# Kernel tuning notes

Measured on AMD Instinct MI355X. Metric: run time of the kernel, lower is better.

Reference implementation:

```python
import jax, jax.numpy as jnp
import numpy as np

N, E, DIN, D, H = 10000, 160000, 256, 64, 8
HC = D * H  # 512

def _p(key, shape, fan_in):
    return jax.random.normal(key, shape, dtype=jnp.float32) * (1.0 / np.sqrt(fan_in))

def setup_inputs() -> dict:
    key = jax.random.key(0)
    k = iter(jax.random.split(key, 64))
    inp = {}
    inp['x'] = jax.random.normal(next(k), (N, DIN), dtype=jnp.float32)
    inp['edge_index'] = jax.random.randint(next(k), (2, E), 0, N, dtype=jnp.int64)
    inp['Wp'] = _p(next(k), (DIN, D), DIN); inp['bp'] = jnp.zeros((D,), jnp.float32)
    # layer 0: in=D -> H*D
    for nm in ['Wq0', 'Wk0', 'Wv0', 'Ws0']:
        inp[nm] = _p(next(k), (D, HC), D)
    for nm in ['bq0', 'bk0', 'bv0', 'bs0']:
        inp[nm] = jnp.zeros((HC,), jnp.float32)
    # layers 1..4 stacked: in=HC -> HC
    for nm in ['Wq', 'Wk', 'Wv', 'Ws']:
        inp[nm] = _p(next(k), (4, HC, HC), HC)
    for nm in ['bq', 'bk', 'bv', 'bs']:
        inp[nm] = jnp.zeros((4, HC), jnp.float32)
    # final conv: in=HC -> D, heads=1, concat=False
    for nm in ['Wqf', 'Wkf', 'Wvf', 'Wsf']:
        inp[nm] = _p(next(k), (HC, D), HC)
    for nm in ['bqf', 'bkf', 'bvf', 'bsf']:
        inp[nm] = jnp.zeros((D,), jnp.float32)
    inp['Wc1'] = _p(next(k), (D, D // 2), D); inp['bc1'] = jnp.zeros((D // 2,), jnp.float32)
    inp['Wc2'] = _p(next(k), (D // 2, 2), D // 2); inp['bc2'] = jnp.zeros((2,), jnp.float32)
    return inp

def _tconv(x, src, dst, Wq, bq, Wk, bk, Wv, bv, Ws, bs, heads, concat):
    n = x.shape[0]
    c = Wq.shape[1] // heads
    q = (x @ Wq + bq).reshape(n, heads, c)
    kk = (x @ Wk + bk).reshape(n, heads, c)
    v = (x @ Wv + bv).reshape(n, heads, c)
    scale = 1.0 / jnp.sqrt(jnp.asarray(c, x.dtype))
    alpha = jnp.einsum('ehc,ehc->eh', q[dst], kk[src]) * scale  # [E,H]
    amax = jax.ops.segment_max(alpha, dst, num_segments=n)
    ex = jnp.exp(alpha - amax[dst])
    denom = jax.ops.segment_sum(ex, dst, num_segments=n)
    w = ex / denom[dst]  # segment softmax over incoming edges
    agg = jax.ops.segment_sum(w[:, :, None] * v[src], dst, num_segments=n)  # [N,H,C]
    skip = x @ Ws + bs
    if concat:
        return agg.reshape(n, heads * c) + skip
    return agg.mean(axis=1) + skip

def reference(x, edge_index, Wp, bp, Wq0, bq0, Wk0, bk0, Wv0, bv0, Ws0, bs0,
              Wq, bq, Wk, bk, Wv, bv, Ws, bs,
              Wqf, bqf, Wkf, bkf, Wvf, bvf, Wsf, bsf,
              Wc1, bc1, Wc2, bc2):
    src, dst = edge_index[0], edge_index[1]
    h = x @ Wp + bp
    h = jax.nn.relu(_tconv(h, src, dst, Wq0, bq0, Wk0, bk0, Wv0, bv0, Ws0, bs0, H, True))
    for l in range(4):
        h = jax.nn.relu(_tconv(h, src, dst, Wq[l], bq[l], Wk[l], bk[l], Wv[l], bv[l], Ws[l], bs[l], H, True))
    h = _tconv(h, src, dst, Wqf, bqf, Wkf, bkf, Wvf, bvf, Wsf, bsf, 1, False)
    g = h.mean(axis=0, keepdims=True)  # batch=None path: [1,D]
    logits = jax.nn.relu(g @ Wc1 + bc1) @ Wc2 + bc2
    return logits
```

## Files before the change

kernel.cpp:

```cpp
#include <hip/hip_runtime.h>
#include <hip/hip_bf16.h>
#include <cstddef>
#include <cstdint>

static inline int cdiv(int a, int b) { return (a + b - 1) / b; }

typedef short short8v __attribute__((ext_vector_type(8)));
typedef float float4v __attribute__((ext_vector_type(4)));

__device__ inline unsigned short f2b(float f) {
    union { float f; unsigned u; } x; x.f = f;
    unsigned u = x.u;
    return (unsigned short)((u + 0x7fff + ((u >> 16) & 1)) >> 16);
}

__device__ inline float lo2f(unsigned u) { union { unsigned x; float f; } c; c.x = u << 16; return c.f; }
__device__ inline float hi2f(unsigned u) { union { unsigned x; float f; } c; c.x = u & 0xffff0000u; return c.f; }
__device__ inline float b2f(unsigned short b) {
    union { unsigned u; float f; } x; x.u = ((unsigned)b) << 16;
    return x.f;
}

__device__ __forceinline__ void u4tof8(uint4 u, float* f) {
    f[0] = lo2f(u.x); f[1] = hi2f(u.x); f[2] = lo2f(u.y); f[3] = hi2f(u.y);
    f[4] = lo2f(u.z); f[5] = hi2f(u.z); f[6] = lo2f(u.w); f[7] = hi2f(u.w);
}

__device__ __forceinline__ void gload_lds16(const unsigned short* g, unsigned short* lds) {
    __builtin_amdgcn_global_load_lds(
        (const __attribute__((address_space(1))) unsigned int*)g,
        (__attribute__((address_space(3))) unsigned int*)lds, 16, 0, 0);
}


__global__ void count_kernel(const int* __restrict__ ei, int* __restrict__ indeg, int E) {
    int e = blockIdx.x * blockDim.x + threadIdx.x;
    if (e < E) atomicAdd(&indeg[ei[E + e]], 1);
}

__global__ void scan_kernel(const int* __restrict__ indeg, int* __restrict__ offs, int n) {
    __shared__ int tmp[1024];
    __shared__ int carry_s;
    int t = threadIdx.x;
    if (t == 0) { carry_s = 0; offs[0] = 0; }
    __syncthreads();
    for (int base = 0; base < n; base += 1024) {
        int i = base + t;
        int v = (i < n) ? indeg[i] : 0;
        tmp[t] = v;
        __syncthreads();
        for (int d = 1; d < 1024; d <<= 1) {
            int add = (t >= d) ? tmp[t - d] : 0;
            __syncthreads();
            tmp[t] += add;
            __syncthreads();
        }
        if (i < n) offs[i + 1] = carry_s + tmp[t];
        __syncthreads();
        if (t == 0) carry_s += tmp[1023];
        __syncthreads();
    }
}

__global__ void fill_kernel(const int* __restrict__ ei, const int* __restrict__ offs,
                            int* __restrict__ cursor, int* __restrict__ csrc, int E) {
    int e = blockIdx.x * blockDim.x + threadIdx.x;
    if (e < E) {
        int d = ei[E + e];
        int s = ei[e];
        int pos = atomicAdd(&cursor[d], 1);
        csrc[offs[d] + pos] = s;
    }
}


__global__ void f2b_kernel(const float* __restrict__ in, unsigned short* __restrict__ out, int n4) {
    int stride = gridDim.x * blockDim.x;
    for (int i = blockIdx.x * blockDim.x + threadIdx.x; i < n4; i += stride) {
        float4 v = reinterpret_cast<const float4*>(in)[i];
        ushort4 o;
        o.x = f2b(v.x); o.y = f2b(v.y); o.z = f2b(v.z); o.w = f2b(v.w);
        reinterpret_cast<ushort4*>(out)[i] = o;
    }
}

__global__ void transpose_b16_kernel(const float* __restrict__ Wq, const float* __restrict__ Wk,
                                     const float* __restrict__ Wv, const float* __restrict__ Ws,
                                     unsigned short* __restrict__ out) {
    const int K = 512, Nc = 512;
    int z = blockIdx.z;
    int which = z & 3;
    const float* W = (which == 0) ? Wq : (which == 1) ? Wk : (which == 2) ? Wv : Ws;
    W += (size_t)(z >> 2) * K * Nc;
    unsigned short* Wt = out + (size_t)z * K * Nc;
    __shared__ float t[32][33];
    int k0 = blockIdx.x * 32, c0 = blockIdx.y * 32;
    int tx = threadIdx.x, ty = threadIdx.y;
    #pragma unroll
    for (int i = 0; i < 32; i += 8) t[ty + i][tx] = W[(size_t)(k0 + ty + i) * Nc + c0 + tx];
    __syncthreads();
    #pragma unroll
    for (int i = 0; i < 32; i += 8) Wt[(size_t)(c0 + ty + i) * K + k0 + tx] = f2b(t[tx][ty + i]);
}

struct SmallT {
    const float* src[9];
    unsigned short* dst[9];
    int rows[9];
    int cols[9];
};

__global__ void transpose_small_kernel(SmallT p) {
    int mat = blockIdx.y;
    int rows = p.rows[mat], cols = p.cols[mat];
    int tilesC = cols >> 5;
    int tiles = (rows >> 5) * tilesC;
    if ((int)blockIdx.x >= tiles) return;
    int tr = blockIdx.x / tilesC, tc = blockIdx.x % tilesC;
    const float* src = p.src[mat];
    unsigned short* dst = p.dst[mat];
    __shared__ float t[32][33];
    int r0 = tr * 32, c0 = tc * 32;
    int tx = threadIdx.x, ty = threadIdx.y;
    #pragma unroll
    for (int i = 0; i < 32; i += 8) t[ty + i][tx] = src[(size_t)(r0 + ty + i) * cols + c0 + tx];
    __syncthreads();
    #pragma unroll
    for (int i = 0; i < 32; i += 8) dst[(size_t)(c0 + ty + i) * rows + r0 + tx] = f2b(t[tx][ty + i]);
}


struct GemmPtrs {
    const unsigned short* B[4];
    const float* bias[4];
    void* C[4];
    int bf16[4];
};

__global__ __launch_bounds__(256) void mfma_gemm4(const unsigned short* __restrict__ A,
                                                  GemmPtrs p, int M, int nb) {
    __shared__ unsigned short As[128 * 32];
    __shared__ unsigned short Bs[128 * 32];
    int i = blockIdx.x;
    int wk = (nb & 7) ? i : ((i & 7) * (nb >> 3) + (i >> 3));
    int xt = wk >> 4, yt = wk & 15;
    int row0 = xt * 128;
    int wsel = yt >> 2;
    int col0 = (yt & 3) * 128;
    const unsigned short* Bt = p.B[wsel];

    int tid = threadIdx.x;
    int lane = tid & 63;
    int w = tid >> 6;
    int wr = w >> 1, wc = w & 1;
    float4v acc[4][4] = {};

    int c0i = w * 2;
    int srow = c0i * 16 + (lane >> 2);
    int scol = (lane & 3) * 8;

    const unsigned short* Abase = A + (size_t)row0 * 512;
    const unsigned short* Bbase = Bt + (size_t)col0 * 512;

    for (int k0 = 0; k0 < 512; k0 += 32) {
        gload_lds16(Abase + (size_t)srow * 512 + k0 + scol, &As[c0i * 512]);
        gload_lds16(Abase + (size_t)(srow + 16) * 512 + k0 + scol, &As[(c0i + 1) * 512]);
        gload_lds16(Bbase + (size_t)srow * 512 + k0 + scol, &Bs[c0i * 512]);
        gload_lds16(Bbase + (size_t)(srow + 16) * 512 + k0 + scol, &Bs[(c0i + 1) * 512]);
        __syncthreads();
        int r16 = lane & 15;
        int kc = (lane >> 4) * 8;
        short8v af[4], bf[4];
        #pragma unroll
        for (int mi = 0; mi < 4; ++mi)
            af[mi] = *reinterpret_cast<const short8v*>(&As[(wr * 64 + mi * 16 + r16) * 32 + kc]);
        #pragma unroll
        for (int nj = 0; nj < 4; ++nj)
            bf[nj] = *reinterpret_cast<const short8v*>(&Bs[(wc * 64 + nj * 16 + r16) * 32 + kc]);
        #pragma unroll
        for (int mi = 0; mi < 4; ++mi)
            #pragma unroll
            for (int nj = 0; nj < 4; ++nj)
                acc[mi][nj] = __builtin_amdgcn_mfma_f32_16x16x32_bf16(af[mi], bf[nj], acc[mi][nj], 0, 0, 0);
        __syncthreads();
    }

    const float* bias = p.bias[wsel];
    int outbf = p.bf16[wsel];
    float* Cf = (float*)p.C[wsel];
    unsigned short* Cb = (unsigned short*)p.C[wsel];
    int crow_base = row0 + wr * 64 + (lane >> 4) * 4;
    int ccol_base = col0 + wc * 64 + (lane & 15);
    #pragma unroll
    for (int mi = 0; mi < 4; ++mi) {
        #pragma unroll
        for (int r = 0; r < 4; ++r) {
            int grow = crow_base + mi * 16 + r;
            if (grow >= M) continue;
            #pragma unroll
            for (int nj = 0; nj < 4; ++nj) {
                int gcol = ccol_base + nj * 16;
                float val = acc[mi][nj][r] + bias[gcol];
                if (outbf) Cb[(size_t)grow * 512 + gcol] = f2b(val);
                else       Cf[(size_t)grow * 512 + gcol] = val;
            }
        }
    }
}


__global__ __launch_bounds__(256) void mfma_flex(const unsigned short* __restrict__ A,
                                                 GemmPtrs p, int M, int K, int Nc) {
    __shared__ unsigned short As[128][40];
    __shared__ unsigned short Bs[64][40];
    int tid = threadIdx.x;
    int lane = tid & 63;
    int w = tid >> 6;
    int row0 = blockIdx.x * 128;
    int nb = Nc >> 6;
    int wsel = blockIdx.y / nb;
    int col0 = (blockIdx.y % nb) * 64;
    const unsigned short* Bt = p.B[wsel];

    float4v acc[2][4] = {};

    int ra = tid >> 1;
    int ca = (tid & 1) * 16;
    int rb = tid >> 2;
    int cb = (tid & 3) * 8;

    for (int k0 = 0; k0 < K; k0 += 32) {
        {
            int grow = row0 + ra;
            uint4 a0 = make_uint4(0u, 0u, 0u, 0u), a1 = make_uint4(0u, 0u, 0u, 0u);
            if (grow < M) {
                a0 = *reinterpret_cast<const uint4*>(&A[(size_t)grow * K + k0 + ca]);
                a1 = *reinterpret_cast<const uint4*>(&A[(size_t)grow * K + k0 + ca + 8]);
            }
            *reinterpret_cast<uint4*>(&As[ra][ca]) = a0;
            *reinterpret_cast<uint4*>(&As[ra][ca + 8]) = a1;
            uint4 bv = *reinterpret_cast<const uint4*>(&Bt[(size_t)(col0 + rb) * K + k0 + cb]);
            *reinterpret_cast<uint4*>(&Bs[rb][cb]) = bv;
        }
        __syncthreads();
        short8v af[2], bf[4];
        int r16 = lane & 15;
        int kc = (lane >> 4) * 8;
        #pragma unroll
        for (int mi = 0; mi < 2; ++mi)
            af[mi] = *reinterpret_cast<const short8v*>(&As[w * 32 + mi * 16 + r16][kc]);
        #pragma unroll
        for (int nj = 0; nj < 4; ++nj)
            bf[nj] = *reinterpret_cast<const short8v*>(&Bs[nj * 16 + r16][kc]);
        #pragma unroll
        for (int mi = 0; mi < 2; ++mi)
            #pragma unroll
            for (int nj = 0; nj < 4; ++nj)
                acc[mi][nj] = __builtin_amdgcn_mfma_f32_16x16x32_bf16(af[mi], bf[nj], acc[mi][nj], 0, 0, 0);
        __syncthreads();
    }

    const float* bias = p.bias[wsel];
    int outbf = p.bf16[wsel];
    float* Cf = (float*)p.C[wsel];
    unsigned short* Cb = (unsigned short*)p.C[wsel];
    int crow_base = row0 + w * 32 + (lane >> 4) * 4;
    int ccol_base = col0 + (lane & 15);
    #pragma unroll
    for (int mi = 0; mi < 2; ++mi) {
        #pragma unroll
        for (int r = 0; r < 4; ++r) {
            int grow = crow_base + mi * 16 + r;
            if (grow >= M) continue;
            #pragma unroll
            for (int nj = 0; nj < 4; ++nj) {
                int gcol = ccol_base + nj * 16;
                float val = acc[mi][nj][r] + bias[gcol];
                if (outbf) Cb[(size_t)grow * Nc + gcol] = f2b(val);
                else       Cf[(size_t)grow * Nc + gcol] = val;
            }
        }
    }
}


__global__ __launch_bounds__(256) void agg8_kernel(const unsigned short* __restrict__ q,
                                                   const unsigned short* __restrict__ kb,
                                                   const unsigned short* __restrict__ vb,
                                                   const unsigned short* __restrict__ skip,
                                                   const int* __restrict__ offs, const int* __restrict__ csrc,
                                                   unsigned short* __restrict__ outb, int N) {
    int lane = threadIdx.x & 63;
    int node = blockIdx.x * (blockDim.x >> 6) + (threadIdx.x >> 6);
    if (node >= N) return;

    size_t rbase = (size_t)node * 512 + lane * 8;
    float qv[8];
    u4tof8(*reinterpret_cast<const uint4*>(&q[rbase]), qv);

    int e0 = offs[node], e1 = offs[node + 1];
    float m = -3.4e38f, wsum = 0.f;
    float accv[8] = {};

    int s = e0;
    for (; s + 2 <= e1; s += 2) {
        int src0 = csrc[s], src1 = csrc[s + 1];
        size_t b0 = (size_t)src0 * 512 + lane * 8;
        size_t b1 = (size_t)src1 * 512 + lane * 8;
        uint4 k0 = *reinterpret_cast<const uint4*>(&kb[b0]);
        uint4 k1 = *reinterpret_cast<const uint4*>(&kb[b1]);
        uint4 v0 = *reinterpret_cast<const uint4*>(&vb[b0]);
        uint4 v1 = *reinterpret_cast<const uint4*>(&vb[b1]);
        float kk0[8], kk1[8], vv0[8], vv1[8];
        u4tof8(k0, kk0); u4tof8(k1, kk1); u4tof8(v0, vv0); u4tof8(v1, vv1);
        float d0 = 0.f, d1 = 0.f;
        #pragma unroll
        for (int j = 0; j < 8; ++j) { d0 += qv[j] * kk0[j]; d1 += qv[j] * kk1[j]; }
        d0 += __shfl_xor(d0, 1); d1 += __shfl_xor(d1, 1);
        d0 += __shfl_xor(d0, 2); d1 += __shfl_xor(d1, 2);
        d0 += __shfl_xor(d0, 4); d1 += __shfl_xor(d1, 4);
        float a0 = d0 * 0.125f, a1 = d1 * 0.125f;
        float mnew = fmaxf(m, fmaxf(a0, a1));
        float corr = __expf(m - mnew);
        float x0 = __expf(a0 - mnew);
        float x1 = __expf(a1 - mnew);
        wsum = wsum * corr + x0 + x1;
        #pragma unroll
        for (int j = 0; j < 8; ++j) accv[j] = accv[j] * corr + x0 * vv0[j] + x1 * vv1[j];
        m = mnew;
    }
    if (s < e1) {
        int src0 = csrc[s];
        size_t b0 = (size_t)src0 * 512 + lane * 8;
        float kk0[8], vv0[8];
        u4tof8(*reinterpret_cast<const uint4*>(&kb[b0]), kk0);
        u4tof8(*reinterpret_cast<const uint4*>(&vb[b0]), vv0);
        float d0 = 0.f;
        #pragma unroll
        for (int j = 0; j < 8; ++j) d0 += qv[j] * kk0[j];
        d0 += __shfl_xor(d0, 1);
        d0 += __shfl_xor(d0, 2);
        d0 += __shfl_xor(d0, 4);
        float a0 = d0 * 0.125f;
        float mnew = fmaxf(m, a0);
        float corr = __expf(m - mnew);
        float x0 = __expf(a0 - mnew);
        wsum = wsum * corr + x0;
        #pragma unroll
        for (int j = 0; j < 8; ++j) accv[j] = accv[j] * corr + x0 * vv0[j];
        m = mnew;
    }

    float inv = (e1 > e0) ? (1.0f / wsum) : 0.f;
    float sk[8];
    u4tof8(*reinterpret_cast<const uint4*>(&skip[rbase]), sk);
    ushort4 o0, o1;
    o0.x = f2b(fmaxf(sk[0] + accv[0] * inv, 0.f));
    o0.y = f2b(fmaxf(sk[1] + accv[1] * inv, 0.f));
    o0.z = f2b(fmaxf(sk[2] + accv[2] * inv, 0.f));
    o0.w = f2b(fmaxf(sk[3] + accv[3] * inv, 0.f));
    o1.x = f2b(fmaxf(sk[4] + accv[4] * inv, 0.f));
    o1.y = f2b(fmaxf(sk[5] + accv[5] * inv, 0.f));
    o1.z = f2b(fmaxf(sk[6] + accv[6] * inv, 0.f));
    o1.w = f2b(fmaxf(sk[7] + accv[7] * inv, 0.f));
    *reinterpret_cast<ushort4*>(&outb[rbase]) = o0;
    *reinterpret_cast<ushort4*>(&outb[rbase + 4]) = o1;
}


__global__ __launch_bounds__(256) void aggf_kernel(const unsigned short* __restrict__ q,
                                                   const unsigned short* __restrict__ kb,
                                                   const unsigned short* __restrict__ vb,
                                                   const int* __restrict__ offs, const int* __restrict__ csrc,
                                                   float* __restrict__ out, int N) {
    const int HC = 64;
    int lane = threadIdx.x & 63;
    int node = blockIdx.x * (blockDim.x >> 6) + (threadIdx.x >> 6);
    if (node >= N) return;
    int g = lane >> 4;
    int r = lane & 15;

    size_t qbase = (size_t)node * HC + 4 * r;
    ushort4 q4u = *reinterpret_cast<const ushort4*>(&q[qbase]);
    float q4[4] = {b2f(q4u.x), b2f(q4u.y), b2f(q4u.z), b2f(q4u.w)};

    int e0 = offs[node], e1 = offs[node + 1];
    float m = -3.4e38f, wsum = 0.f;
    float accv[4] = {0.f, 0.f, 0.f, 0.f};

    int nIt = (e1 - e0 + 3) >> 2;
    for (int it = 0; it < nIt; ++it) {
        int s = e0 + it * 4 + g;
        bool valid = s < e1;
        int src = csrc[valid ? s : (e1 - 1)];
        size_t base = (size_t)src * HC + 4 * r;
        ushort4 k4 = *reinterpret_cast<const ushort4*>(&kb[base]);
        float d = q4[0] * b2f(k4.x) + q4[1] * b2f(k4.y) + q4[2] * b2f(k4.z) + q4[3] * b2f(k4.w);
        d += __shfl_xor(d, 1);
        d += __shfl_xor(d, 2);
        d += __shfl_xor(d, 4);
        d += __shfl_xor(d, 8);
        float alpha = valid ? d * 0.125f : -3.4e38f;
        float am = fmaxf(alpha, __shfl_xor(alpha, 16));
        am = fmaxf(am, __shfl_xor(am, 32));
        float mnew = fmaxf(m, am);
        float corr = __expf(m - mnew);
        float ex = __expf(alpha - mnew);
        ushort4 v4 = *reinterpret_cast<const ushort4*>(&vb[base]);
        wsum = wsum * corr + ex;
        accv[0] = accv[0] * corr + ex * b2f(v4.x);
        accv[1] = accv[1] * corr + ex * b2f(v4.y);
        accv[2] = accv[2] * corr + ex * b2f(v4.z);
        accv[3] = accv[3] * corr + ex * b2f(v4.w);
        m = mnew;
    }

    #pragma unroll
    for (int off = 16; off <= 32; off <<= 1) {
        wsum += __shfl_xor(wsum, off);
        #pragma unroll
        for (int j = 0; j < 4; ++j) accv[j] += __shfl_xor(accv[j], off);
    }

    if (g == 0) {
        float inv = (e1 > e0) ? (1.0f / wsum) : 0.f;
        float4 o = *reinterpret_cast<const float4*>(&out[qbase]);
        o.x += accv[0] * inv;
        o.y += accv[1] * inv;
        o.z += accv[2] * inv;
        o.w += accv[3] * inv;
        *reinterpret_cast<float4*>(&out[qbase]) = o;
    }
}


__global__ void pool_kernel(const float* __restrict__ hin, float* __restrict__ g, int N) {
    int dim = blockIdx.x;
    float s = 0.f;
    for (int i = threadIdx.x; i < N; i += blockDim.x) s += hin[(size_t)i * 64 + dim];
    __shared__ float red[256];
    red[threadIdx.x] = s;
    __syncthreads();
    for (int d = 128; d >= 1; d >>= 1) {
        if ((int)threadIdx.x < d) red[threadIdx.x] += red[threadIdx.x + d];
        __syncthreads();
    }
    if (threadIdx.x == 0) g[dim] = red[0] / (float)N;
}

__global__ void mlp_kernel(const float* __restrict__ g, const float* __restrict__ Wc1,
                           const float* __restrict__ bc1, const float* __restrict__ Wc2,
                           const float* __restrict__ bc2, float* __restrict__ out) {
    __shared__ float gs[64];
    __shared__ float h1[32];
    int t = threadIdx.x;
    if (t < 64) gs[t] = g[t];
    __syncthreads();
    if (t < 32) {
        float s = bc1[t];
        for (int i = 0; i < 64; ++i) s += gs[i] * Wc1[i * 32 + t];
        h1[t] = fmaxf(s, 0.f);
    }
    __syncthreads();
    if (t < 2) {
        float s = bc2[t];
        for (int i = 0; i < 32; ++i) s += h1[i] * Wc2[i * 2 + t];
        out[t] = s;
    }
}


extern "C" void kernel_launch(void* const* d_in, const int* in_sizes, int n_in,
                              void* d_out, int out_size, void* d_ws, size_t ws_size,
                              hipStream_t stream) {
    const float* x   = (const float*)d_in[0];
    const int*   ei  = (const int*)d_in[1];
    const float* Wp  = (const float*)d_in[2];
    const float* bp  = (const float*)d_in[3];
    const float* Wq0 = (const float*)d_in[4];
    const float* Wk0 = (const float*)d_in[5];
    const float* Wv0 = (const float*)d_in[6];
    const float* Ws0 = (const float*)d_in[7];
    const float* bq0 = (const float*)d_in[8];
    const float* bk0 = (const float*)d_in[9];
    const float* bv0 = (const float*)d_in[10];
    const float* bs0 = (const float*)d_in[11];
    const float* Wq  = (const float*)d_in[12];
    const float* Wk  = (const float*)d_in[13];
    const float* Wv  = (const float*)d_in[14];
    const float* Ws  = (const float*)d_in[15];
    const float* bq  = (const float*)d_in[16];
    const float* bk  = (const float*)d_in[17];
    const float* bv  = (const float*)d_in[18];
    const float* bs  = (const float*)d_in[19];
    const float* Wqf = (const float*)d_in[20];
    const float* Wkf = (const float*)d_in[21];
    const float* Wvf = (const float*)d_in[22];
    const float* Wsf = (const float*)d_in[23];
    const float* bqf = (const float*)d_in[24];
    const float* bkf = (const float*)d_in[25];
    const float* bvf = (const float*)d_in[26];
    const float* bsf = (const float*)d_in[27];
    const float* Wc1 = (const float*)d_in[28];
    const float* bc1 = (const float*)d_in[29];
    const float* Wc2 = (const float*)d_in[30];
    const float* bc2 = (const float*)d_in[31];

    const int N = in_sizes[0] / 256;
    const int E = in_sizes[1] / 2;
    const int HC = 512;

    size_t NB = (size_t)N * HC;
    const size_t WSMALL = 64 * 256 + 8 * 512 * 64;
    size_t need = 6 * NB * sizeof(unsigned short)
                + (size_t)16 * 512 * 512 * sizeof(unsigned short)
                + WSMALL * sizeof(unsigned short)
                + NB * sizeof(float)
                + (size_t)(2 * N + 1 + E) * sizeof(int)
                + 64 * sizeof(float) + 4096;
    if (ws_size < need) return;

    unsigned short* h0    = (unsigned short*)d_ws;
    unsigned short* h1    = h0 + NB;
    unsigned short* qb16  = h1 + NB;
    unsigned short* kb    = qb16 + NB;
    unsigned short* vb    = kb + NB;
    unsigned short* skipb = vb + NB;
    unsigned short* wt16  = skipb + NB;
    unsigned short* wsm   = wt16 + (size_t)16 * 512 * 512;
    uintptr_t pa = (uintptr_t)(wsm + WSMALL);
    pa = (pa + 255) & ~(uintptr_t)255;
    float* hf32 = (float*)pa;
    int* offs   = (int*)(hf32 + NB);
    int* cursor = offs + (N + 1);
    int* csrc   = cursor + N;
    float* gbuf = (float*)(csrc + E);
    unsigned short* xb = qb16;

    hipMemsetAsync(cursor, 0, sizeof(int) * N, stream);
    count_kernel<<<cdiv(E, 256), 256, 0, stream>>>(ei, cursor, E);
    scan_kernel<<<1, 1024, 0, stream>>>(cursor, offs, N);
    hipMemsetAsync(cursor, 0, sizeof(int) * N, stream);
    fill_kernel<<<cdiv(E, 256), 256, 0, stream>>>(ei, offs, cursor, csrc, E);

    transpose_b16_kernel<<<dim3(16, 16, 16), dim3(32, 8), 0, stream>>>(Wq, Wk, Wv, Ws, wt16);
    {
        SmallT st;
        unsigned short* wp_t = wsm;
        unsigned short* w0_t = wsm + 64 * 256;
        unsigned short* wf_t = w0_t + 4 * 512 * 64;
        st.src[0] = Wp;  st.dst[0] = wp_t; st.rows[0] = 256; st.cols[0] = 64;
        const float* w0s[4] = {Wq0, Wk0, Wv0, Ws0};
        const float* wfs[4] = {Wqf, Wkf, Wvf, Wsf};
        for (int i = 0; i < 4; ++i) {
            st.src[1 + i] = w0s[i]; st.dst[1 + i] = w0_t + i * 512 * 64;
            st.rows[1 + i] = 64; st.cols[1 + i] = 512;
            st.src[5 + i] = wfs[i]; st.dst[5 + i] = wf_t + i * 64 * 512;
            st.rows[5 + i] = 512; st.cols[5 + i] = 64;
        }
        transpose_small_kernel<<<dim3(32, 9), dim3(32, 8), 0, stream>>>(st);
    }

    f2b_kernel<<<1280, 256, 0, stream>>>(x, xb, N * 256 / 4);
    {
        GemmPtrs gp;
        gp.B[0] = wsm; gp.bias[0] = bp; gp.C[0] = h0; gp.bf16[0] = 1;
        gp.B[1] = gp.B[2] = gp.B[3] = wsm; gp.bias[1] = gp.bias[2] = gp.bias[3] = bp;
        gp.C[1] = gp.C[2] = gp.C[3] = h0; gp.bf16[1] = gp.bf16[2] = gp.bf16[3] = 1;
        mfma_flex<<<dim3(cdiv(N, 128), 1), 256, 0, stream>>>(xb, gp, N, 256, 64);
    }

    {
        GemmPtrs gp;
        unsigned short* w0_t = wsm + 64 * 256;
        gp.B[0] = w0_t + 0 * 512 * 64; gp.bias[0] = bq0; gp.C[0] = qb16;  gp.bf16[0] = 1;
        gp.B[1] = w0_t + 1 * 512 * 64; gp.bias[1] = bk0; gp.C[1] = kb;    gp.bf16[1] = 1;
        gp.B[2] = w0_t + 2 * 512 * 64; gp.bias[2] = bv0; gp.C[2] = vb;    gp.bf16[2] = 1;
        gp.B[3] = w0_t + 3 * 512 * 64; gp.bias[3] = bs0; gp.C[3] = skipb; gp.bf16[3] = 1;
        mfma_flex<<<dim3(cdiv(N, 128), 4 * 8), 256, 0, stream>>>(h0, gp, N, 64, 512);
    }
    agg8_kernel<<<cdiv(N, 4), 256, 0, stream>>>(qb16, kb, vb, skipb, offs, csrc, h1, N);

    unsigned short* hcur = h1;
    unsigned short* hnext = h0;
    int gx = cdiv(N, 128);
    for (int l = 0; l < 4; ++l) {
        GemmPtrs gp;
        gp.B[0] = wt16 + (size_t)(l * 4 + 0) * 512 * 512;
        gp.B[1] = wt16 + (size_t)(l * 4 + 1) * 512 * 512;
        gp.B[2] = wt16 + (size_t)(l * 4 + 2) * 512 * 512;
        gp.B[3] = wt16 + (size_t)(l * 4 + 3) * 512 * 512;
        gp.bias[0] = bq + l * HC;
        gp.bias[1] = bk + l * HC;
        gp.bias[2] = bv + l * HC;
        gp.bias[3] = bs + l * HC;
        gp.C[0] = qb16; gp.C[1] = kb; gp.C[2] = vb; gp.C[3] = skipb;
        gp.bf16[0] = 1; gp.bf16[1] = 1; gp.bf16[2] = 1; gp.bf16[3] = 1;
        mfma_gemm4<<<gx * 16, 256, 0, stream>>>(hcur, gp, N, gx * 16);
        agg8_kernel<<<cdiv(N, 4), 256, 0, stream>>>(qb16, kb, vb, skipb, offs, csrc, hnext, N);
        { unsigned short* t = hcur; hcur = hnext; hnext = t; }
    }

    {
        GemmPtrs gp;
        unsigned short* wf_t = wsm + 64 * 256 + 4 * 512 * 64;
        gp.B[0] = wf_t + 0 * 64 * 512; gp.bias[0] = bqf; gp.C[0] = qb16; gp.bf16[0] = 1;
        gp.B[1] = wf_t + 1 * 64 * 512; gp.bias[1] = bkf; gp.C[1] = kb;   gp.bf16[1] = 1;
        gp.B[2] = wf_t + 2 * 64 * 512; gp.bias[2] = bvf; gp.C[2] = vb;   gp.bf16[2] = 1;
        gp.B[3] = wf_t + 3 * 64 * 512; gp.bias[3] = bsf; gp.C[3] = hf32; gp.bf16[3] = 0;
        mfma_flex<<<dim3(cdiv(N, 128), 4), 256, 0, stream>>>(hcur, gp, N, 512, 64);
    }
    aggf_kernel<<<cdiv(N, 4), 256, 0, stream>>>(qb16, kb, vb, offs, csrc, hf32, N);

    pool_kernel<<<64, 256, 0, stream>>>(hf32, gbuf, N);
    mlp_kernel<<<1, 64, 0, stream>>>(gbuf, Wc1, bc1, Wc2, bc2, (float*)d_out);
}
```

Before: 595.9 us.

## Load GEMM fragments directly from global into registers with prefetch, drop LDS staging

The mfma_gemm4 kernel no longer stages A/B tiles through LDS with barriers. Each lane now loads its MFMA fragments straight from global memory, double-buffering the next k-slice in registers while the current MFMAs run. This removes the two barriers and the LDS round trip per k-step. In exchange, data shared between waves is loaded redundantly from global/L2, and the loads are strided 16-byte accesses per row, which are less coalesced.

```diff
diff --git a/kernel.cpp b/kernel.cpp
--- a/kernel.cpp
+++ b/kernel.cpp
@@ -24,12 +24,6 @@
 __device__ __forceinline__ void u4tof8(uint4 u, float* f) {
     f[0] = lo2f(u.x); f[1] = hi2f(u.x); f[2] = lo2f(u.y); f[3] = hi2f(u.y);
     f[4] = lo2f(u.z); f[5] = hi2f(u.z); f[6] = lo2f(u.w); f[7] = hi2f(u.w);
-}
-
-__device__ __forceinline__ void gload_lds16(const unsigned short* g, unsigned short* lds) {
-    __builtin_amdgcn_global_load_lds(
-        (const __attribute__((address_space(1))) unsigned int*)g,
-        (__attribute__((address_space(3))) unsigned int*)lds, 16, 0, 0);
 }
 
 
@@ -139,8 +133,6 @@
 
 __global__ __launch_bounds__(256) void mfma_gemm4(const unsigned short* __restrict__ A,
                                                   GemmPtrs p, int M, int nb) {
-    __shared__ unsigned short As[128 * 32];
-    __shared__ unsigned short Bs[128 * 32];
     int i = blockIdx.x;
     int wk = (nb & 7) ? i : ((i & 7) * (nb >> 3) + (i >> 3));
     int xt = wk >> 4, yt = wk & 15;
@@ -153,36 +145,44 @@
     int lane = tid & 63;
     int w = tid >> 6;
     int wr = w >> 1, wc = w & 1;
+    int r16 = lane & 15;
+    int kc = (lane >> 4) * 8;
+
     float4v acc[4][4] = {};
 
-    int c0i = w * 2;
-    int srow = c0i * 16 + (lane >> 2);
-    int scol = (lane & 3) * 8;
-
-    const unsigned short* Abase = A + (size_t)row0 * 512;
-    const unsigned short* Bbase = Bt + (size_t)col0 * 512;
+    const unsigned short* Ap[4];
+    const unsigned short* Bp[4];
+    #pragma unroll
+    for (int t = 0; t < 4; ++t) {
+        int ra = row0 + wr * 64 + t * 16 + r16;
+        if (ra >= M) ra = M - 1;
+        Ap[t] = A + (size_t)ra * 512 + kc;
+        Bp[t] = Bt + (size_t)(col0 + wc * 64 + t * 16 + r16) * 512 + kc;
+    }
+
+    short8v a_[4], b_[4], an[4], bn[4];
+    #pragma unroll
+    for (int t = 0; t < 4; ++t) {
+        a_[t] = *reinterpret_cast<const short8v*>(Ap[t]);
+        b_[t] = *reinterpret_cast<const short8v*>(Bp[t]);
+    }
 
     for (int k0 = 0; k0 < 512; k0 += 32) {
-        gload_lds16(Abase + (size_t)srow * 512 + k0 + scol, &As[c0i * 512]);
-        gload_lds16(Abase + (size_t)(srow + 16) * 512 + k0 + scol, &As[(c0i + 1) * 512]);
-        gload_lds16(Bbase + (size_t)srow * 512 + k0 + scol, &Bs[c0i * 512]);
-        gload_lds16(Bbase + (size_t)(srow + 16) * 512 + k0 + scol, &Bs[(c0i + 1) * 512]);
-        __syncthreads();
-        int r16 = lane & 15;
-        int kc = (lane >> 4) * 8;
-        short8v af[4], bf[4];
-        #pragma unroll
-        for (int mi = 0; mi < 4; ++mi)
-            af[mi] = *reinterpret_cast<const short8v*>(&As[(wr * 64 + mi * 16 + r16) * 32 + kc]);
-        #pragma unroll
-        for (int nj = 0; nj < 4; ++nj)
-            bf[nj] = *reinterpret_cast<const short8v*>(&Bs[(wc * 64 + nj * 16 + r16) * 32 + kc]);
+        int nxt = k0 + 32;
+        if (nxt < 512) {
+            #pragma unroll
+            for (int t = 0; t < 4; ++t) {
+                an[t] = *reinterpret_cast<const short8v*>(Ap[t] + nxt);
+                bn[t] = *reinterpret_cast<const short8v*>(Bp[t] + nxt);
+            }
+        }
         #pragma unroll
         for (int mi = 0; mi < 4; ++mi)
             #pragma unroll
             for (int nj = 0; nj < 4; ++nj)
-                acc[mi][nj] = __builtin_amdgcn_mfma_f32_16x16x32_bf16(af[mi], bf[nj], acc[mi][nj], 0, 0, 0);
-        __syncthreads();
+                acc[mi][nj] = __builtin_amdgcn_mfma_f32_16x16x32_bf16(a_[mi], b_[nj], acc[mi][nj], 0, 0, 0);
+        #pragma unroll
+        for (int t = 0; t < 4; ++t) { a_[t] = an[t]; b_[t] = bn[t]; }
     }
 
     const float* bias = p.bias[wsel];
```

New measurement: 829.1 us. 39.1% more time.

## Store K/V head-major and aggregate per head with four edges per wave

Applied to the files above, without the earlier changes.

The GEMM epilogues now write K and V in head-major layout ([head][node][64]). The attention aggregation is split so each wave handles one (node, head) pair, processing four edges in parallel across 16-lane groups. Per-head K/V tables are smaller, so gathers should get better cache locality per head, and there are eight times as many blocks for parallelism. In exchange, Q and skip reads are repeated per head, the epilogue stores become strided, and extra shuffles are needed to merge the four edge groups.

```diff
diff --git a/kernel.cpp b/kernel.cpp
--- a/kernel.cpp
+++ b/kernel.cpp
@@ -135,10 +135,11 @@
     const float* bias[4];
     void* C[4];
     int bf16[4];
+    int hm[4];
 };
 
 __global__ __launch_bounds__(256) void mfma_gemm4(const unsigned short* __restrict__ A,
-                                                  GemmPtrs p, int M, int nb) {
+                                                  GemmPtrs p, int M, int nb, int kvN) {
     __shared__ unsigned short As[128 * 32];
     __shared__ unsigned short Bs[128 * 32];
     int i = blockIdx.x;
@@ -187,10 +188,12 @@
 
     const float* bias = p.bias[wsel];
     int outbf = p.bf16[wsel];
+    int hm = p.hm[wsel];
     float* Cf = (float*)p.C[wsel];
     unsigned short* Cb = (unsigned short*)p.C[wsel];
     int crow_base = row0 + wr * 64 + (lane >> 4) * 4;
     int ccol_base = col0 + wc * 64 + (lane & 15);
+    int headbase = (col0 + wc * 64) >> 6;
     #pragma unroll
     for (int mi = 0; mi < 4; ++mi) {
         #pragma unroll
@@ -201,8 +204,13 @@
             for (int nj = 0; nj < 4; ++nj) {
                 int gcol = ccol_base + nj * 16;
                 float val = acc[mi][nj][r] + bias[gcol];
-                if (outbf) Cb[(size_t)grow * 512 + gcol] = f2b(val);
-                else       Cf[(size_t)grow * 512 + gcol] = val;
+                if (hm) {
+                    Cb[((size_t)headbase * kvN + grow) * 64 + (gcol & 63)] = f2b(val);
+                } else if (outbf) {
+                    Cb[(size_t)grow * 512 + gcol] = f2b(val);
+                } else {
+                    Cf[(size_t)grow * 512 + gcol] = val;
+                }
             }
         }
     }
@@ -210,7 +218,7 @@
 
 
 __global__ __launch_bounds__(256) void mfma_flex(const unsigned short* __restrict__ A,
-                                                 GemmPtrs p, int M, int K, int Nc) {
+                                                 GemmPtrs p, int M, int K, int Nc, int kvN) {
     __shared__ unsigned short As[128][40];
     __shared__ unsigned short Bs[64][40];
     int tid = threadIdx.x;
@@ -262,10 +270,12 @@
 
     const float* bias = p.bias[wsel];
     int outbf = p.bf16[wsel];
+    int hm = p.hm[wsel];
     float* Cf = (float*)p.C[wsel];
     unsigned short* Cb = (unsigned short*)p.C[wsel];
     int crow_base = row0 + w * 32 + (lane >> 4) * 4;
     int ccol_base = col0 + (lane & 15);
+    int headbase = col0 >> 6;
     #pragma unroll
     for (int mi = 0; mi < 2; ++mi) {
         #pragma unroll
@@ -276,95 +286,87 @@
             for (int nj = 0; nj < 4; ++nj) {
                 int gcol = ccol_base + nj * 16;
                 float val = acc[mi][nj][r] + bias[gcol];
-                if (outbf) Cb[(size_t)grow * Nc + gcol] = f2b(val);
-                else       Cf[(size_t)grow * Nc + gcol] = val;
+                if (hm) {
+                    Cb[((size_t)headbase * kvN + grow) * 64 + (gcol & 63)] = f2b(val);
+                } else if (outbf) {
+                    Cb[(size_t)grow * Nc + gcol] = f2b(val);
+                } else {
+                    Cf[(size_t)grow * Nc + gcol] = val;
+                }
             }
         }
     }
 }
 
 
-__global__ __launch_bounds__(256) void agg8_kernel(const unsigned short* __restrict__ q,
-                                                   const unsigned short* __restrict__ kb,
-                                                   const unsigned short* __restrict__ vb,
-                                                   const unsigned short* __restrict__ skip,
-                                                   const int* __restrict__ offs, const int* __restrict__ csrc,
-                                                   unsigned short* __restrict__ outb, int N) {
+__global__ __launch_bounds__(256) void agg8h_kernel(const unsigned short* __restrict__ q,
+                                                    const unsigned short* __restrict__ kb,
+                                                    const unsigned short* __restrict__ vb,
+                                                    const unsigned short* __restrict__ skip,
+                                                    const int* __restrict__ offs, const int* __restrict__ csrc,
+                                                    unsigned short* __restrict__ outb, int N) {
+    int head = blockIdx.x & 7;
+    int node = (blockIdx.x >> 3) * (blockDim.x >> 6) + (threadIdx.x >> 6);
+    if (node >= N) return;
     int lane = threadIdx.x & 63;
-    int node = blockIdx.x * (blockDim.x >> 6) + (threadIdx.x >> 6);
-    if (node >= N) return;
-
-    size_t rbase = (size_t)node * 512 + lane * 8;
-    float qv[8];
-    u4tof8(*reinterpret_cast<const uint4*>(&q[rbase]), qv);
+    int g = lane >> 4;
+    int r = lane & 15;
+
+    size_t qoff = (size_t)node * 512 + head * 64 + 4 * r;
+    ushort4 q4u = *reinterpret_cast<const ushort4*>(&q[qoff]);
+    float q4[4] = {b2f(q4u.x), b2f(q4u.y), b2f(q4u.z), b2f(q4u.w)};
+
+    const unsigned short* kh = kb + (size_t)head * N * 64;
+    const unsigned short* vh = vb + (size_t)head * N * 64;
 
     int e0 = offs[node], e1 = offs[node + 1];
     float m = -3.4e38f, wsum = 0.f;
-    float accv[8] = {};
-
-    int s = e0;
-    for (; s + 2 <= e1; s += 2) {
-        int src0 = csrc[s], src1 = csrc[s + 1];
-        size_t b0 = (size_t)src0 * 512 + lane * 8;
-        size_t b1 = (size_t)src1 * 512 + lane * 8;
-        uint4 k0 = *reinterpret_cast<const uint4*>(&kb[b0]);
-        uint4 k1 = *reinterpret_cast<const uint4*>(&kb[b1]);
-        uint4 v0 = *reinterpret_cast<const uint4*>(&vb[b0]);
-        uint4 v1 = *reinterpret_cast<const uint4*>(&vb[b1]);
-        float kk0[8], kk1[8], vv0[8], vv1[8];
-        u4tof8(k0, kk0); u4tof8(k1, kk1); u4tof8(v0, vv0); u4tof8(v1, vv1);
-        float d0 = 0.f, d1 = 0.f;
-        #pragma unroll
-        for (int j = 0; j < 8; ++j) { d0 += qv[j] * kk0[j]; d1 += qv[j] * kk1[j]; }
-        d0 += __shfl_xor(d0, 1); d1 += __shfl_xor(d1, 1);
-        d0 += __shfl_xor(d0, 2); d1 += __shfl_xor(d1, 2);
-        d0 += __shfl_xor(d0, 4); d1 += __shfl_xor(d1, 4);
-        float a0 = d0 * 0.125f, a1 = d1 * 0.125f;
-        float mnew = fmaxf(m, fmaxf(a0, a1));
+    float accv[4] = {0.f, 0.f, 0.f, 0.f};
+
+    int nIt = (e1 - e0 + 3) >> 2;
+    for (int it = 0; it < nIt; ++it) {
+        int s = e0 + it * 4 + g;
+        bool valid = s < e1;
+        int src = csrc[valid ? s : (e1 - 1)];
+        size_t base = (size_t)src * 64 + 4 * r;
+        ushort4 k4 = *reinterpret_cast<const ushort4*>(&kh[base]);
+        float d = q4[0] * b2f(k4.x) + q4[1] * b2f(k4.y) + q4[2] * b2f(k4.z) + q4[3] * b2f(k4.w);
+        d += __shfl_xor(d, 1);
+        d += __shfl_xor(d, 2);
+        d += __shfl_xor(d, 4);
+        d += __shfl_xor(d, 8);
+        float alpha = valid ? d * 0.125f : -3.4e38f;
+        float am = fmaxf(alpha, __shfl_xor(alpha, 16));
+        am = fmaxf(am, __shfl_xor(am, 32));
+        float mnew = fmaxf(m, am);
         float corr = __expf(m - mnew);
-        float x0 = __expf(a0 - mnew);
-        float x1 = __expf(a1 - mnew);
-        wsum = wsum * corr + x0 + x1;
-        #pragma unroll
-        for (int j = 0; j < 8; ++j) accv[j] = accv[j] * corr + x0 * vv0[j] + x1 * vv1[j];
+        float ex = __expf(alpha - mnew);
+        ushort4 v4 = *reinterpret_cast<const ushort4*>(&vh[base]);
+        wsum = wsum * corr + ex;
+        accv[0] = accv[0] * corr + ex * b2f(v4.x);
+        accv[1] = accv[1] * corr + ex * b2f(v4.y);
+        accv[2] = accv[2] * corr + ex * b2f(v4.z);
+        accv[3] = accv[3] * corr + ex * b2f(v4.w);
         m = mnew;
     }
-    if (s < e1) {
-        int src0 = csrc[s];
-        size_t b0 = (size_t)src0 * 512 + lane * 8;
-        float kk0[8], vv0[8];
-        u4tof8(*reinterpret_cast<const uint4*>(&kb[b0]), kk0);
-        u4tof8(*reinterpret_cast<const uint4*>(&vb[b0]), vv0);
-        float d0 = 0.f;
-        #pragma unroll
-        for (int j = 0; j < 8; ++j) d0 += qv[j] * kk0[j];
-        d0 += __shfl_xor(d0, 1);
-        d0 += __shfl_xor(d0, 2);
-        d0 += __shfl_xor(d0, 4);
-        float a0 = d0 * 0.125f;
-        float mnew = fmaxf(m, a0);
-        float corr = __expf(m - mnew);
-        float x0 = __expf(a0 - mnew);
-        wsum = wsum * corr + x0;
-        #pragma unroll
-        for (int j = 0; j < 8; ++j) accv[j] = accv[j] * corr + x0 * vv0[j];
-        m = mnew;
-    }
-
-    float inv = (e1 > e0) ? (1.0f / wsum) : 0.f;
-    float sk[8];
-    u4tof8(*reinterpret_cast<const uint4*>(&skip[rbase]), sk);
-    ushort4 o0, o1;
-    o0.x = f2b(fmaxf(sk[0] + accv[0] * inv, 0.f));
-    o0.y = f2b(fmaxf(sk[1] + accv[1] * inv, 0.f));
-    o0.z = f2b(fmaxf(sk[2] + accv[2] * inv, 0.f));
-    o0.w = f2b(fmaxf(sk[3] + accv[3] * inv, 0.f));
-    o1.x = f2b(fmaxf(sk[4] + accv[4] * inv, 0.f));
-    o1.y = f2b(fmaxf(sk[5] + accv[5] * inv, 0.f));
-    o1.z = f2b(fmaxf(sk[6] + accv[6] * inv, 0.f));
-    o1.w = f2b(fmaxf(sk[7] + accv[7] * inv, 0.f));
-    *reinterpret_cast<ushort4*>(&outb[rbase]) = o0;
-    *reinterpret_cast<ushort4*>(&outb[rbase + 4]) = o1;
+
+    #pragma unroll
+    for (int off = 16; off <= 32; off <<= 1) {
+        wsum += __shfl_xor(wsum, off);
+        #pragma unroll
+        for (int j = 0; j < 4; ++j) accv[j] += __shfl_xor(accv[j], off);
+    }
+
+    if (g == 0) {
+        float inv = (e1 > e0) ? (1.0f / wsum) : 0.f;
+        ushort4 sku = *reinterpret_cast<const ushort4*>(&skip[qoff]);
+        ushort4 o;
+        o.x = f2b(fmaxf(b2f(sku.x) + accv[0] * inv, 0.f));
+        o.y = f2b(fmaxf(b2f(sku.y) + accv[1] * inv, 0.f));
+        o.z = f2b(fmaxf(b2f(sku.z) + accv[2] * inv, 0.f));
+        o.w = f2b(fmaxf(b2f(sku.w) + accv[3] * inv, 0.f));
+        *reinterpret_cast<ushort4*>(&outb[qoff]) = o;
+    }
 }
 
 
@@ -564,22 +566,22 @@
     f2b_kernel<<<1280, 256, 0, stream>>>(x, xb, N * 256 / 4);
     {
         GemmPtrs gp;
-        gp.B[0] = wsm; gp.bias[0] = bp; gp.C[0] = h0; gp.bf16[0] = 1;
-        gp.B[1] = gp.B[2] = gp.B[3] = wsm; gp.bias[1] = gp.bias[2] = gp.bias[3] = bp;
-        gp.C[1] = gp.C[2] = gp.C[3] = h0; gp.bf16[1] = gp.bf16[2] = gp.bf16[3] = 1;
-        mfma_flex<<<dim3(cdiv(N, 128), 1), 256, 0, stream>>>(xb, gp, N, 256, 64);
+        for (int j = 0; j < 4; ++j) {
+            gp.B[j] = wsm; gp.bias[j] = bp; gp.C[j] = h0; gp.bf16[j] = 1; gp.hm[j] = 0;
+        }
+        mfma_flex<<<dim3(cdiv(N, 128), 1), 256, 0, stream>>>(xb, gp, N, 256, 64, N);
     }
 
     {
         GemmPtrs gp;
         unsigned short* w0_t = wsm + 64 * 256;
-        gp.B[0] = w0_t + 0 * 512 * 64; gp.bias[0] = bq0; gp.C[0] = qb16;  gp.bf16[0] = 1;
-        gp.B[1] = w0_t + 1 * 512 * 64; gp.bias[1] = bk0; gp.C[1] = kb;    gp.bf16[1] = 1;
-        gp.B[2] = w0_t + 2 * 512 * 64; gp.bias[2] = bv0; gp.C[2] = vb;    gp.bf16[2] = 1;
-        gp.B[3] = w0_t + 3 * 512 * 64; gp.bias[3] = bs0; gp.C[3] = skipb; gp.bf16[3] = 1;
-        mfma_flex<<<dim3(cdiv(N, 128), 4 * 8), 256, 0, stream>>>(h0, gp, N, 64, 512);
-    }
-    agg8_kernel<<<cdiv(N, 4), 256, 0, stream>>>(qb16, kb, vb, skipb, offs, csrc, h1, N);
+        gp.B[0] = w0_t + 0 * 512 * 64; gp.bias[0] = bq0; gp.C[0] = qb16;  gp.bf16[0] = 1; gp.hm[0] = 0;
+        gp.B[1] = w0_t + 1 * 512 * 64; gp.bias[1] = bk0; gp.C[1] = kb;    gp.bf16[1] = 1; gp.hm[1] = 1;
+        gp.B[2] = w0_t + 2 * 512 * 64; gp.bias[2] = bv0; gp.C[2] = vb;    gp.bf16[2] = 1; gp.hm[2] = 1;
+        gp.B[3] = w0_t + 3 * 512 * 64; gp.bias[3] = bs0; gp.C[3] = skipb; gp.bf16[3] = 1; gp.hm[3] = 0;
+        mfma_flex<<<dim3(cdiv(N, 128), 4 * 8), 256, 0, stream>>>(h0, gp, N, 64, 512, N);
+    }
+    agg8h_kernel<<<cdiv(N, 4) * 8, 256, 0, stream>>>(qb16, kb, vb, skipb, offs, csrc, h1, N);
 
     unsigned short* hcur = h1;
     unsigned short* hnext = h0;
@@ -596,19 +598,20 @@
         gp.bias[3] = bs + l * HC;
         gp.C[0] = qb16; gp.C[1] = kb; gp.C[2] = vb; gp.C[3] = skipb;
         gp.bf16[0] = 1; gp.bf16[1] = 1; gp.bf16[2] = 1; gp.bf16[3] = 1;
-        mfma_gemm4<<<gx * 16, 256, 0, stream>>>(hcur, gp, N, gx * 16);
-        agg8_kernel<<<cdiv(N, 4), 256, 0, stream>>>(qb16, kb, vb, skipb, offs, csrc, hnext, N);
+        gp.hm[0] = 0; gp.hm[1] = 1; gp.hm[2] = 1; gp.hm[3] = 0;
+        mfma_gemm4<<<gx * 16, 256, 0, stream>>>(hcur, gp, N, gx * 16, N);
+        agg8h_kernel<<<cdiv(N, 4) * 8, 256, 0, stream>>>(qb16, kb, vb, skipb, offs, csrc, hnext, N);
         { unsigned short* t = hcur; hcur = hnext; hnext = t; }
     }
 
     {
         GemmPtrs gp;
         unsigned short* wf_t = wsm + 64 * 256 + 4 * 512 * 64;
-        gp.B[0] = wf_t + 0 * 64 * 512; gp.bias[0] = bqf; gp.C[0] = qb16; gp.bf16[0] = 1;
-        gp.B[1] = wf_t + 1 * 64 * 512; gp.bias[1] = bkf; gp.C[1] = kb;   gp.bf16[1] = 1;
-        gp.B[2] = wf_t + 2 * 64 * 512; gp.bias[2] = bvf; gp.C[2] = vb;   gp.bf16[2] = 1;
-        gp.B[3] = wf_t + 3 * 64 * 512; gp.bias[3] = bsf; gp.C[3] = hf32; gp.bf16[3] = 0;
-        mfma_flex<<<dim3(cdiv(N, 128), 4), 256, 0, stream>>>(hcur, gp, N, 512, 64);
+        gp.B[0] = wf_t + 0 * 64 * 512; gp.bias[0] = bqf; gp.C[0] = qb16; gp.bf16[0] = 1; gp.hm[0] = 0;
+        gp.B[1] = wf_t + 1 * 64 * 512; gp.bias[1] = bkf; gp.C[1] = kb;   gp.bf16[1] = 1; gp.hm[1] = 0;
+        gp.B[2] = wf_t + 2 * 64 * 512; gp.bias[2] = bvf; gp.C[2] = vb;   gp.bf16[2] = 1; gp.hm[2] = 0;
+        gp.B[3] = wf_t + 3 * 64 * 512; gp.bias[3] = bsf; gp.C[3] = hf32; gp.bf16[3] = 0; gp.hm[3] = 0;
+        mfma_flex<<<dim3(cdiv(N, 128), 4), 256, 0, stream>>>(hcur, gp, N, 512, 64, N);
     }
     aggf_kernel<<<cdiv(N, 4), 256, 0, stream>>>(qb16, kb, vb, offs, csrc, hf32, N);
 
```

After: 649.4 us. 1.09x slower.
